# Kernel tuning notes

Hardware: AMD Instinct MI355X
Metric: run time of the kernel (lower is better)

## Reference

```python
import jax, jax.numpy as jnp
import numpy as np

B, S, E = 8, 2048, 2048   # batch, items, embedding_width
H, Dh = 16, 128           # head_width, head_embeddings (E = H*Dh)
M = 1024                  # memory_width


def setup_inputs() -> dict:
    key = jax.random.key(0)
    ks = jax.random.split(key, 9)
    scale_e = 1.0 / np.sqrt(E)
    scale_d = 1.0 / np.sqrt(Dh)
    return {
        "tensor": jax.random.normal(ks[0], (B, S, E), dtype=jnp.float32),
        # Query: Linear(E -> [H, Dh])
        "Wq": jax.random.normal(ks[1], (E, H, Dh), dtype=jnp.float32) * scale_e,
        "bq": jnp.zeros((H, Dh), dtype=jnp.float32),
        # trainable key/value banks + calibration (kaiming-uniform-like init)
        "key_params": (jax.random.uniform(ks[2], (H, M, Dh), dtype=jnp.float32) * 2 - 1) * np.sqrt(6.0 / Dh),
        "calibration": jnp.zeros((H, M, Dh), dtype=jnp.float32),
        "value": (jax.random.uniform(ks[3], (H, M, Dh), dtype=jnp.float32) * 2 - 1) * np.sqrt(6.0 / Dh),
        # Dehead: Linear([H, Dh] -> E)
        "Wd": jax.random.normal(ks[4], (H, Dh, E), dtype=jnp.float32) * scale_d,
        "bd": jnp.zeros((E,), dtype=jnp.float32),
    }


def reference(tensor, Wq, bq, key_params, calibration, value, Wd, bd):
    # query projection to heads: (B,S,E) -> (B,H,S,Dh) (fuses transpose(-2,-3))
    q = jnp.einsum("bse,ehd->bhsd", tensor, Wq) + bq[:, None, :]
    # eval-mode dropout is identity; key = KeyParameters + CalibrationBuffer
    k = key_params + calibration                      # (H,M,Dh)
    # scores scaled by sqrt(FULL embedding width), per the source
    score = jnp.einsum("bhsd,hmd->bhsm", q, k) / jnp.sqrt(jnp.float32(E))
    attn = jax.nn.softmax(score, axis=-1)             # (B,H,S,M)
    out = jnp.einsum("bhsm,hmd->bhsd", attn, value)   # (B,H,S,Dh)
    # dehead: (B,H,S,Dh) -> (B,S,E)
    return jnp.einsum("bhsd,hde->bse", out, Wd) + bd
```

## Files before the change

kernel.cpp:

```cpp
#include <hip/hip_runtime.h>
#include <stdint.h>

#define B_ 8
#define S_ 2048
#define E_ 2048
#define H_ 16
#define DH_ 128
#define M_ 1024
#define K_ 2048

typedef float f32x4 __attribute__((ext_vector_type(4)));
typedef float f32x16 __attribute__((ext_vector_type(16)));
typedef __bf16 bf16x8 __attribute__((ext_vector_type(8)));
typedef unsigned short ushort8 __attribute__((ext_vector_type(8)));
typedef unsigned short ushort4v __attribute__((ext_vector_type(4)));
typedef unsigned int uint4v __attribute__((ext_vector_type(4)));
typedef float float4v __attribute__((ext_vector_type(4)));

static __device__ __forceinline__ unsigned short f2bf(float f) {
  unsigned int u = __builtin_bit_cast(unsigned int, f);
  u += 0x7fffu + ((u >> 16) & 1u);
  return (unsigned short)(u >> 16);
}

static __device__ __forceinline__ float exp2f_fast(float x) {
#if __has_builtin(__builtin_amdgcn_exp2f)
  return __builtin_amdgcn_exp2f(x);
#else
  return __expf(x * 0.6931471805599453f);
#endif
}

static __device__ __forceinline__ f32x4 mfma16(ushort8 a, ushort8 b, f32x4 c) {
  return __builtin_amdgcn_mfma_f32_16x16x32_bf16(
      __builtin_bit_cast(bf16x8, a), __builtin_bit_cast(bf16x8, b), c, 0, 0, 0);
}

static __device__ __forceinline__ f32x16 mfma32(ushort8 a, ushort8 b, f32x16 c) {
  return __builtin_amdgcn_mfma_f32_32x32x16_bf16(
      __builtin_bit_cast(bf16x8, a), __builtin_bit_cast(bf16x8, b), c, 0, 0, 0);
}

static __device__ __forceinline__ void gload_lds16(const void* g, void* l) {
  __builtin_amdgcn_global_load_lds(
      (const __attribute__((address_space(1))) unsigned int*)g,
      (__attribute__((address_space(3))) unsigned int*)l, 16, 0, 0);
}


__global__ void cvt_bf16(const float* __restrict__ in, unsigned short* __restrict__ out, int n4) {
  int i = blockIdx.x * blockDim.x + threadIdx.x;
  int stride = gridDim.x * blockDim.x;
  for (; i < n4; i += stride) {
    float4v v = ((const float4v*)in)[i];
    ushort4v o;
    o[0] = f2bf(v[0]); o[1] = f2bf(v[1]); o[2] = f2bf(v[2]); o[3] = f2bf(v[3]);
    ((ushort4v*)out)[i] = o;
  }
}

__global__ void addcvt_bf16(const float* __restrict__ a, const float* __restrict__ b,
                            unsigned short* __restrict__ out, int n4) {
  int i = blockIdx.x * blockDim.x + threadIdx.x;
  int stride = gridDim.x * blockDim.x;
  for (; i < n4; i += stride) {
    float4v va = ((const float4v*)a)[i];
    float4v vb = ((const float4v*)b)[i];
    ushort4v o;
    o[0] = f2bf(va[0] + vb[0]); o[1] = f2bf(va[1] + vb[1]);
    o[2] = f2bf(va[2] + vb[2]); o[3] = f2bf(va[3] + vb[3]);
    ((ushort4v*)out)[i] = o;
  }
}

__global__ __launch_bounds__(256) void transpose_cvt(const float* __restrict__ in,
                                                     unsigned short* __restrict__ out,
                                                     int R, int C) {
  __shared__ float t[64][65];
  const int tx = threadIdx.x & 63, ty = threadIdx.x >> 6;
  const size_t base = (size_t)blockIdx.z * R * C;
  const int r0 = blockIdx.y * 64, c0 = blockIdx.x * 64;
#pragma unroll
  for (int i = 0; i < 64; i += 4)
    t[i + ty][tx] = in[base + (size_t)(r0 + i + ty) * C + (c0 + tx)];
  __syncthreads();
#pragma unroll
  for (int i = 0; i < 64; i += 4)
    out[base + (size_t)(c0 + i + ty) * R + (r0 + tx)] = f2bf(t[tx][i + ty]);
}

template <int EPI>
__global__ __launch_bounds__(512, 2) void gemm8p(const unsigned short* __restrict__ A,
                                                 const unsigned short* __restrict__ BT,
                                                 const float* __restrict__ bias,
                                                 void* __restrict__ Cout) {
  __shared__ __align__(16) unsigned short a_lds[2][2][8192];
  __shared__ __align__(16) unsigned short b_lds[2][2][8192];
  const int tid = threadIdx.x;
  const int w = tid >> 6, lane = tid & 63;
  const int l16 = lane & 15, l4 = lane >> 4;
  const int wr = w >> 2, wc = w & 3;
  const int bid = blockIdx.x;
  const int n0 = (bid & 7) << 8;
  const int m0 = (bid >> 3) << 8;

  const int rp0 = tid >> 3, gg0 = tid & 7, s0 = gg0 ^ (rp0 & 7);
  const int srow = rp0 * 2 + (s0 >> 2), sg = s0 & 3;
  const unsigned short* pA = A + (size_t)(m0 + srow) * K_ + sg * 8;
  const unsigned short* pB = BT + (size_t)(n0 + srow) * K_ + sg * 8;
  const int laneG = ((l16 >> 1) * 8 + (((l16 & 1) * 4 + l4) ^ ((l16 >> 1) & 7))) * 8;

  f32x4 acc[8][4];
#pragma unroll
  for (int i = 0; i < 8; ++i)
#pragma unroll
    for (int j = 0; j < 4; ++j) acc[i][j] = (f32x4)(0.f);

  ushort8 aF[4], bF[4];

#define STG(dst, srcp, T, kh)                                                \
  do {                                                                       \
    const unsigned short* s_ = (srcp) + (T) * 64 + (kh) * 32;                \
    gload_lds16(s_, &(dst)[tid * 8]);                                        \
    gload_lds16(s_ + (size_t)128 * K_, &(dst)[(512 + tid) * 8]);             \
  } while (0)

#define LDA(mg, buf, ks)                                                     \
  do {                                                                       \
    _Pragma("unroll") for (int mf = 0; mf < 4; ++mf)                         \
      aF[mf] = *(const ushort8*)&a_lds[buf][ks]                              \
          [(wr * 512 + ((mg) * 4 + mf) * 64) * 8 + laneG];                   \
  } while (0)

#define LDB(buf, ks)                                                         \
  do {                                                                       \
    _Pragma("unroll") for (int nf = 0; nf < 4; ++nf)                         \
      bF[nf] = *(const ushort8*)&b_lds[buf][ks]                              \
          [(wc * 256 + nf * 64) * 8 + laneG];                                \
  } while (0)

#define MM(mg)                                                               \
  do {                                                                       \
    __builtin_amdgcn_s_setprio(1);                                           \
    _Pragma("unroll") for (int mf = 0; mf < 4; ++mf)                         \
      _Pragma("unroll") for (int nf = 0; nf < 4; ++nf)                       \
        acc[(mg) * 4 + mf][nf] = mfma16(aF[mf], bF[nf], acc[(mg) * 4 + mf][nf]); \
    __builtin_amdgcn_s_setprio(0);                                           \
  } while (0)

#define NOVM ((void)0)
#define VMC6 asm volatile("s_waitcnt vmcnt(6)" ::: "memory")
#define VMC0 asm volatile("s_waitcnt vmcnt(0)" ::: "memory")

#define PHASE(mg, ks, buf, LOADB, STAGE, VM)                                 \
  do {                                                                       \
    if (LOADB) { LDB(buf, ks); }                                             \
    LDA(mg, buf, ks);                                                        \
    STAGE;                                                                   \
    __builtin_amdgcn_s_barrier();                                            \
    asm volatile("s_waitcnt lgkmcnt(0)" ::: "memory");                       \
    __builtin_amdgcn_sched_barrier(0);                                       \
    MM(mg);                                                                  \
    VM;                                                                      \
    __builtin_amdgcn_s_barrier();                                            \
  } while (0)

  STG(a_lds[0][0], pA, 0, 0);
  STG(b_lds[0][0], pB, 0, 0);
  STG(a_lds[0][1], pA, 0, 1);
  STG(b_lds[0][1], pB, 0, 1);
  STG(b_lds[1][0], pB, 1, 0);
  STG(a_lds[1][0], pA, 1, 0);
  STG(b_lds[1][1], pB, 1, 1);
  __builtin_amdgcn_sched_barrier(0);
  VMC6;
  __builtin_amdgcn_s_barrier();
  __builtin_amdgcn_sched_barrier(0);

#pragma unroll 1
  for (int i = 0; i < 15; ++i) {
    const int t1 = 2 * i + 1, t2 = 2 * i + 2, t3 = 2 * i + 3;
    PHASE(0, 0, 0, 1, STG(a_lds[1][1], pA, t1, 1), NOVM);
    PHASE(1, 0, 0, 0, STG(b_lds[0][0], pB, t2, 0), NOVM);
    PHASE(1, 1, 0, 1, STG(a_lds[0][0], pA, t2, 0), NOVM);
    PHASE(0, 1, 0, 0, STG(b_lds[0][1], pB, t2, 1), VMC6);
    PHASE(0, 0, 1, 1, STG(a_lds[0][1], pA, t2, 1), NOVM);
    PHASE(1, 0, 1, 0, STG(b_lds[1][0], pB, t3, 0), NOVM);
    PHASE(1, 1, 1, 1, STG(a_lds[1][0], pA, t3, 0), NOVM);
    PHASE(0, 1, 1, 0, STG(b_lds[1][1], pB, t3, 1), VMC6);
  }
  PHASE(0, 0, 0, 1, STG(a_lds[1][1], pA, 31, 1), NOVM);
  PHASE(1, 0, 0, 0, NOVM, NOVM);
  PHASE(1, 1, 0, 1, NOVM, NOVM);
  PHASE(0, 1, 0, 0, NOVM, VMC0);
  PHASE(0, 0, 1, 1, NOVM, NOVM);
  PHASE(1, 0, 1, 0, NOVM, NOVM);
  PHASE(1, 1, 1, 1, NOVM, NOVM);
  PHASE(0, 1, 1, 0, NOVM, NOVM);

#undef PHASE
#undef STG
#undef LDA
#undef LDB
#undef MM

#pragma unroll
  for (int mf = 0; mf < 8; ++mf) {
    const int mb = m0 + wr * 128 + mf * 16 + l4 * 4;
#pragma unroll
    for (int nf = 0; nf < 4; ++nf) {
      const int n = n0 + wc * 64 + nf * 16 + l16;
      const float bv = bias[n];
#pragma unroll
      for (int r = 0; r < 4; ++r) {
        const float v = acc[mf][nf][r] + bv;
        const int m = mb + r;
        if (EPI == 0) {
          const int b = m >> 11, s = m & 2047, h = n >> 7, d = n & 127;
          ((unsigned short*)Cout)[(((size_t)(b * 16 + h) << 11) + s) * 128 + d] =
              f2bf(v * 0.031879358f);
        } else {
          ((float*)Cout)[(size_t)m * E_ + n] = v;
        }
      }
    }
  }
}

__global__ __launch_bounds__(512, 2) void attn32(const unsigned short* __restrict__ Qb,
                                                 const unsigned short* __restrict__ Kb,
                                                 const unsigned short* __restrict__ VT,
                                                 unsigned short* __restrict__ Ob) {
  const int bh = blockIdx.x, b = bh >> 4, h = bh & 15;
  const int tid = threadIdx.x, wv = tid >> 6, lane = tid & 63;
  const int l32 = lane & 31, hi = lane >> 5;
  const int s_glob = blockIdx.y * 256 + wv * 32 + l32;

  __shared__ __align__(16) unsigned short k_sm[2][64 * 128];
  __shared__ __align__(16) unsigned short v_sm[2][128 * 64];
  __shared__ float inv_lds[8][32];

  const unsigned short* Kh = Kb + (size_t)h * M_ * DH_;
  const unsigned short* Vh = VT + (size_t)h * DH_ * M_;

  ushort8 qf[8];
  {
    const unsigned short* qrow = Qb + ((size_t)(b * 16 + h) * S_ + s_glob) * DH_ + hi * 8;
#pragma unroll
    for (int dc = 0; dc < 8; ++dc) qf[dc] = *(const ushort8*)(qrow + dc * 16);
  }

  f32x16 oacc[4];
#pragma unroll
  for (int dt = 0; dt < 4; ++dt) oacc[dt] = (f32x16)(0.f);
  float lsum = 0.f;

#define ASTAGE(buf, ch)                                                        \
  do {                                                                         \
    const int m0_ = (ch) << 6;                                                 \
    _Pragma("unroll") for (int j_ = 0; j_ < 2; ++j_) {                         \
      const int t_ = j_ * 512 + tid;                                           \
      const int m_ = t_ >> 4, p_ = t_ & 15;                                    \
      gload_lds16(Kh + (size_t)(m0_ + m_) * DH_ + ((p_ ^ (m_ & 7)) << 3),      \
                  &k_sm[buf][t_ * 8]);                                         \
    }                                                                          \
    _Pragma("unroll") for (int j_ = 0; j_ < 2; ++j_) {                         \
      const int t_ = j_ * 512 + tid;                                           \
      const int d_ = t_ >> 3, p_ = t_ & 7;                                     \
      gload_lds16(Vh + (size_t)d_ * M_ + m0_ + ((p_ ^ (d_ & 7)) << 3),         \
                  &v_sm[buf][t_ * 8]);                                         \
    }                                                                          \
  } while (0)

  int cur = 0;
  ASTAGE(0, 0);
  __syncthreads();

  for (int c = 0; c < 16; ++c) {
    if (c < 15) ASTAGE(cur ^ 1, c + 1);

    f32x16 sacc[2];
    sacc[0] = (f32x16)(0.f);
    sacc[1] = (f32x16)(0.f);
#pragma unroll
    for (int mb = 0; mb < 2; ++mb) {
      const int m_ = mb * 32 + l32;
      const unsigned short* kr = &k_sm[cur][m_ * 128];
      __builtin_amdgcn_s_setprio(1);
#pragma unroll
      for (int dc = 0; dc < 8; ++dc) {
        ushort8 kf = *(const ushort8*)(kr + (((dc * 2 + hi) ^ (m_ & 7)) << 3));
        sacc[mb] = mfma32(kf, qf[dc], sacc[mb]);
      }
      __builtin_amdgcn_s_setprio(0);
    }

#pragma unroll
    for (int mb = 0; mb < 2; ++mb) {
      float pe[16];
#pragma unroll
      for (int r = 0; r < 16; ++r) {
        pe[r] = exp2f_fast(sacc[mb][r]);
        lsum += pe[r];
      }
      ushort8 pa[2];
#pragma unroll
      for (int mk = 0; mk < 2; ++mk) {
        const int o = mk * 8;
        unsigned x0, x1, y0, y1;
        asm("v_cvt_pk_bf16_f32 %0, %1, %2" : "=v"(x0) : "v"(pe[o + 0]), "v"(pe[o + 1]));
        asm("v_cvt_pk_bf16_f32 %0, %1, %2" : "=v"(x1) : "v"(pe[o + 2]), "v"(pe[o + 3]));
        asm("v_cvt_pk_bf16_f32 %0, %1, %2" : "=v"(y0) : "v"(pe[o + 4]), "v"(pe[o + 5]));
        asm("v_cvt_pk_bf16_f32 %0, %1, %2" : "=v"(y1) : "v"(pe[o + 6]), "v"(pe[o + 7]));
        asm("v_permlane32_swap_b32 %0, %1" : "+v"(x0), "+v"(y0));
        asm("v_permlane32_swap_b32 %0, %1" : "+v"(x1), "+v"(y1));
        uint4v pw;
        pw[0] = x0; pw[1] = x1; pw[2] = y0; pw[3] = y1;
        pa[mk] = __builtin_bit_cast(ushort8, pw);
      }
#pragma unroll
      for (int dt = 0; dt < 4; ++dt) {
        const int d_ = dt * 32 + l32;
        const unsigned short* vr = &v_sm[cur][d_ * 64];
        __builtin_amdgcn_s_setprio(1);
#pragma unroll
        for (int mk = 0; mk < 2; ++mk) {
          const int gv = mb * 4 + mk * 2 + hi;
          ushort8 vf = *(const ushort8*)(vr + ((gv ^ (d_ & 7)) << 3));
          oacc[dt] = mfma32(pa[mk], vf, oacc[dt]);
        }
        __builtin_amdgcn_s_setprio(0);
      }
    }
    __syncthreads();
    cur ^= 1;
  }
#undef ASTAGE

  float tot = lsum + __shfl_xor(lsum, 32, 64);
  if (hi == 0) inv_lds[wv][l32] = 1.0f / tot;
#pragma unroll
  for (int r = 0; r < 16; ++r) {
    const int srow = (r & 3) + 8 * (r >> 2) + 4 * hi;
    const float iv = inv_lds[wv][srow];
    unsigned short* orow =
        Ob + ((size_t)b * S_ + (size_t)(blockIdx.y * 256 + wv * 32 + srow)) * (H_ * DH_) +
        h * DH_ + l32;
#pragma unroll
    for (int dt = 0; dt < 4; ++dt) {
      const float val = oacc[dt][r] * iv;
      unsigned u;
      asm("v_cvt_pk_bf16_f32 %0, %1, %2" : "=v"(u) : "v"(val), "v"(val));
      orow[dt * 32] = (unsigned short)u;
    }
  }
}


extern "C" void kernel_launch(void* const* d_in, const int* in_sizes, int n_in,
                              void* d_out, int out_size, void* d_ws, size_t ws_size,
                              hipStream_t stream) {
  const float* X   = (const float*)d_in[0];
  const float* Wq  = (const float*)d_in[1];
  const float* bq  = (const float*)d_in[2];
  const float* Kp  = (const float*)d_in[3];
  const float* Cal = (const float*)d_in[4];
  const float* V   = (const float*)d_in[5];
  const float* Wd  = (const float*)d_in[6];
  const float* bd  = (const float*)d_in[7];

  char* ws = (char*)d_ws;
  unsigned short* Xbf = (unsigned short*)(ws + 0);
  unsigned short* Ob  = Xbf;
  unsigned short* Qb  = (unsigned short*)(ws + 67108864);
  unsigned short* WqT = (unsigned short*)(ws + 134217728);
  unsigned short* WdT = (unsigned short*)(ws + 142606336);
  unsigned short* Kb  = (unsigned short*)(ws + 150994944);
  unsigned short* VT  = (unsigned short*)(ws + 155189248);

  cvt_bf16<<<2048, 256, 0, stream>>>(X, Xbf, (B_ * S_ * E_) / 4);
  addcvt_bf16<<<1024, 256, 0, stream>>>(Kp, Cal, Kb, (H_ * M_ * DH_) / 4);
  transpose_cvt<<<dim3(E_ / 64, E_ / 64, 1), 256, 0, stream>>>(Wq, WqT, E_, H_ * DH_);
  transpose_cvt<<<dim3(E_ / 64, E_ / 64, 1), 256, 0, stream>>>(Wd, WdT, H_ * DH_, E_);
  transpose_cvt<<<dim3(DH_ / 64, M_ / 64, H_), 256, 0, stream>>>(V, VT, M_, DH_);

  gemm8p<0><<<dim3(512), 512, 0, stream>>>(Xbf, WqT, bq, Qb);

  attn32<<<dim3(B_ * H_, S_ / 256), 512, 0, stream>>>(Qb, Kb, VT, Ob);

  gemm8p<1><<<dim3(512), 512, 0, stream>>>(Ob, WdT, bd, (float*)d_out);
}
```

Before: 475.2 us.

## Process two 32-row query tiles per wave in attention to reuse K/V fragments

The attention kernel now runs 256 threads per block, and each wave handles 64 query rows as two 32-row sub-tiles, so every K and V fragment read from LDS feeds two MFMAs instead of one. The K/V staging layout is changed to a fragment-ordered, lane-contiguous arrangement without XOR swizzle, so each lane's 16-byte read is a direct contiguous access. The QK, softmax and PV steps are interleaved per 32-column block. This halves LDS read traffic per MFMA but doubles the accumulator and query registers per wave, which may reduce occupancy or cause spills. Fewer waves per block also leave less latency hiding.

```diff
diff --git a/kernel.cpp b/kernel.cpp
--- a/kernel.cpp
+++ b/kernel.cpp
@@ -227,49 +227,56 @@
   }
 }
 
-__global__ __launch_bounds__(512, 2) void attn32(const unsigned short* __restrict__ Qb,
+__global__ __launch_bounds__(256, 2) void attn64(const unsigned short* __restrict__ Qb,
                                                  const unsigned short* __restrict__ Kb,
                                                  const unsigned short* __restrict__ VT,
                                                  unsigned short* __restrict__ Ob) {
   const int bh = blockIdx.x, b = bh >> 4, h = bh & 15;
   const int tid = threadIdx.x, wv = tid >> 6, lane = tid & 63;
   const int l32 = lane & 31, hi = lane >> 5;
-  const int s_glob = blockIdx.y * 256 + wv * 32 + l32;
-
-  __shared__ __align__(16) unsigned short k_sm[2][64 * 128];
-  __shared__ __align__(16) unsigned short v_sm[2][128 * 64];
-  __shared__ float inv_lds[8][32];
+
+  __shared__ __align__(16) unsigned short k_sm[2][16 * 512];
+  __shared__ __align__(16) unsigned short v_sm[2][16 * 512];
+  __shared__ float inv_lds[4][2][32];
 
   const unsigned short* Kh = Kb + (size_t)h * M_ * DH_;
   const unsigned short* Vh = VT + (size_t)h * DH_ * M_;
 
-  ushort8 qf[8];
-  {
-    const unsigned short* qrow = Qb + ((size_t)(b * 16 + h) * S_ + s_glob) * DH_ + hi * 8;
-#pragma unroll
-    for (int dc = 0; dc < 8; ++dc) qf[dc] = *(const ushort8*)(qrow + dc * 16);
-  }
-
-  f32x16 oacc[4];
-#pragma unroll
-  for (int dt = 0; dt < 4; ++dt) oacc[dt] = (f32x16)(0.f);
-  float lsum = 0.f;
-
-#define ASTAGE(buf, ch)                                                        \
-  do {                                                                         \
-    const int m0_ = (ch) << 6;                                                 \
-    _Pragma("unroll") for (int j_ = 0; j_ < 2; ++j_) {                         \
-      const int t_ = j_ * 512 + tid;                                           \
-      const int m_ = t_ >> 4, p_ = t_ & 15;                                    \
-      gload_lds16(Kh + (size_t)(m0_ + m_) * DH_ + ((p_ ^ (m_ & 7)) << 3),      \
-                  &k_sm[buf][t_ * 8]);                                         \
-    }                                                                          \
-    _Pragma("unroll") for (int j_ = 0; j_ < 2; ++j_) {                         \
-      const int t_ = j_ * 512 + tid;                                           \
-      const int d_ = t_ >> 3, p_ = t_ & 7;                                     \
-      gload_lds16(Vh + (size_t)d_ * M_ + m0_ + ((p_ ^ (d_ & 7)) << 3),         \
-                  &v_sm[buf][t_ * 8]);                                         \
-    }                                                                          \
+  ushort8 qf[2][8];
+#pragma unroll
+  for (int sub = 0; sub < 2; ++sub) {
+    const int srow = blockIdx.y * 256 + wv * 64 + sub * 32 + l32;
+    const unsigned short* qrow = Qb + ((size_t)(b * 16 + h) * S_ + srow) * DH_ + hi * 8;
+#pragma unroll
+    for (int dc = 0; dc < 8; ++dc) qf[sub][dc] = *(const ushort8*)(qrow + dc * 16);
+  }
+
+  f32x16 oacc[2][4];
+#pragma unroll
+  for (int sub = 0; sub < 2; ++sub)
+#pragma unroll
+    for (int dt = 0; dt < 4; ++dt) oacc[sub][dt] = (f32x16)(0.f);
+  float lsum[2] = {0.f, 0.f};
+
+#define ASTAGE(buf, ch)                                                         \
+  do {                                                                          \
+    const int m0c = (ch) << 6;                                                  \
+    _Pragma("unroll") for (int j_ = 0; j_ < 4; ++j_) {                          \
+      const int L_ = j_ * 256 + tid;                                            \
+      const int st_ = L_ >> 6, g_ = L_ & 63;                                    \
+      const int mb_ = st_ >> 3, dc_ = st_ & 7;                                  \
+      const int pt_ = g_ >> 5, rw_ = g_ & 31;                                   \
+      gload_lds16(Kh + (size_t)(m0c + mb_ * 32 + rw_) * DH_ + dc_ * 16 + pt_ * 8, \
+                  &k_sm[buf][L_ * 8]);                                          \
+    }                                                                           \
+    _Pragma("unroll") for (int j_ = 0; j_ < 4; ++j_) {                          \
+      const int L_ = j_ * 256 + tid;                                            \
+      const int st_ = L_ >> 6, g_ = L_ & 63;                                    \
+      const int dt_ = st_ >> 2, mb_ = (st_ >> 1) & 1, mk_ = st_ & 1;            \
+      const int pt_ = g_ >> 5, rw_ = g_ & 31;                                   \
+      gload_lds16(Vh + (size_t)(dt_ * 32 + rw_) * M_ + m0c + mb_ * 32 + mk_ * 16 + pt_ * 8, \
+                  &v_sm[buf][L_ * 8]);                                          \
+    }                                                                           \
   } while (0)
 
   int cur = 0;
@@ -279,81 +286,84 @@
   for (int c = 0; c < 16; ++c) {
     if (c < 15) ASTAGE(cur ^ 1, c + 1);
 
-    f32x16 sacc[2];
-    sacc[0] = (f32x16)(0.f);
-    sacc[1] = (f32x16)(0.f);
 #pragma unroll
     for (int mb = 0; mb < 2; ++mb) {
-      const int m_ = mb * 32 + l32;
-      const unsigned short* kr = &k_sm[cur][m_ * 128];
+      f32x16 sacc0 = (f32x16)(0.f), sacc1 = (f32x16)(0.f);
       __builtin_amdgcn_s_setprio(1);
 #pragma unroll
       for (int dc = 0; dc < 8; ++dc) {
-        ushort8 kf = *(const ushort8*)(kr + (((dc * 2 + hi) ^ (m_ & 7)) << 3));
-        sacc[mb] = mfma32(kf, qf[dc], sacc[mb]);
+        ushort8 kf = *(const ushort8*)&k_sm[cur][((mb * 8 + dc) * 64 + lane) * 8];
+        sacc0 = mfma32(kf, qf[0][dc], sacc0);
+        sacc1 = mfma32(kf, qf[1][dc], sacc1);
+      }
+      __builtin_amdgcn_s_setprio(0);
+
+      ushort8 pa[2][2];
+#pragma unroll
+      for (int sub = 0; sub < 2; ++sub) {
+        float pe[16];
+#pragma unroll
+        for (int r = 0; r < 16; ++r) {
+          pe[r] = exp2f_fast(sub == 0 ? sacc0[r] : sacc1[r]);
+          lsum[sub] += pe[r];
+        }
+#pragma unroll
+        for (int mk = 0; mk < 2; ++mk) {
+          const int o = mk * 8;
+          unsigned x0, x1, y0, y1;
+          asm("v_cvt_pk_bf16_f32 %0, %1, %2" : "=v"(x0) : "v"(pe[o + 0]), "v"(pe[o + 1]));
+          asm("v_cvt_pk_bf16_f32 %0, %1, %2" : "=v"(x1) : "v"(pe[o + 2]), "v"(pe[o + 3]));
+          asm("v_cvt_pk_bf16_f32 %0, %1, %2" : "=v"(y0) : "v"(pe[o + 4]), "v"(pe[o + 5]));
+          asm("v_cvt_pk_bf16_f32 %0, %1, %2" : "=v"(y1) : "v"(pe[o + 6]), "v"(pe[o + 7]));
+          asm("v_permlane32_swap_b32 %0, %1" : "+v"(x0), "+v"(y0));
+          asm("v_permlane32_swap_b32 %0, %1" : "+v"(x1), "+v"(y1));
+          uint4v pw;
+          pw[0] = x0; pw[1] = x1; pw[2] = y0; pw[3] = y1;
+          pa[sub][mk] = __builtin_bit_cast(ushort8, pw);
+        }
+      }
+
+      __builtin_amdgcn_s_setprio(1);
+#pragma unroll
+      for (int dt = 0; dt < 4; ++dt) {
+#pragma unroll
+        for (int mk = 0; mk < 2; ++mk) {
+          ushort8 vf = *(const ushort8*)&v_sm[cur][((dt * 4 + mb * 2 + mk) * 64 + lane) * 8];
+          oacc[0][dt] = mfma32(pa[0][mk], vf, oacc[0][dt]);
+          oacc[1][dt] = mfma32(pa[1][mk], vf, oacc[1][dt]);
+        }
       }
       __builtin_amdgcn_s_setprio(0);
     }
-
-#pragma unroll
-    for (int mb = 0; mb < 2; ++mb) {
-      float pe[16];
-#pragma unroll
-      for (int r = 0; r < 16; ++r) {
-        pe[r] = exp2f_fast(sacc[mb][r]);
-        lsum += pe[r];
-      }
-      ushort8 pa[2];
-#pragma unroll
-      for (int mk = 0; mk < 2; ++mk) {
-        const int o = mk * 8;
-        unsigned x0, x1, y0, y1;
-        asm("v_cvt_pk_bf16_f32 %0, %1, %2" : "=v"(x0) : "v"(pe[o + 0]), "v"(pe[o + 1]));
-        asm("v_cvt_pk_bf16_f32 %0, %1, %2" : "=v"(x1) : "v"(pe[o + 2]), "v"(pe[o + 3]));
-        asm("v_cvt_pk_bf16_f32 %0, %1, %2" : "=v"(y0) : "v"(pe[o + 4]), "v"(pe[o + 5]));
-        asm("v_cvt_pk_bf16_f32 %0, %1, %2" : "=v"(y1) : "v"(pe[o + 6]), "v"(pe[o + 7]));
-        asm("v_permlane32_swap_b32 %0, %1" : "+v"(x0), "+v"(y0));
-        asm("v_permlane32_swap_b32 %0, %1" : "+v"(x1), "+v"(y1));
-        uint4v pw;
-        pw[0] = x0; pw[1] = x1; pw[2] = y0; pw[3] = y1;
-        pa[mk] = __builtin_bit_cast(ushort8, pw);
-      }
+    __syncthreads();
+    cur ^= 1;
+  }
+#undef ASTAGE
+
+#pragma unroll
+  for (int sub = 0; sub < 2; ++sub) {
+    float tot = lsum[sub] + __shfl_xor(lsum[sub], 32, 64);
+    if (hi == 0) inv_lds[wv][sub][l32] = 1.0f / tot;
+  }
+  __builtin_amdgcn_s_barrier();
+#pragma unroll
+  for (int sub = 0; sub < 2; ++sub)
+#pragma unroll
+    for (int r = 0; r < 16; ++r) {
+      const int crow = (r & 3) + 8 * (r >> 2) + 4 * hi;
+      const float iv = inv_lds[wv][sub][crow];
+      unsigned short* orow =
+          Ob + ((size_t)b * S_ + (size_t)(blockIdx.y * 256 + wv * 64 + sub * 32 + crow)) *
+                   (H_ * DH_) +
+          h * DH_ + l32;
 #pragma unroll
       for (int dt = 0; dt < 4; ++dt) {
-        const int d_ = dt * 32 + l32;
-        const unsigned short* vr = &v_sm[cur][d_ * 64];
-        __builtin_amdgcn_s_setprio(1);
-#pragma unroll
-        for (int mk = 0; mk < 2; ++mk) {
-          const int gv = mb * 4 + mk * 2 + hi;
-          ushort8 vf = *(const ushort8*)(vr + ((gv ^ (d_ & 7)) << 3));
-          oacc[dt] = mfma32(pa[mk], vf, oacc[dt]);
-        }
-        __builtin_amdgcn_s_setprio(0);
+        const float val = oacc[sub][dt][r] * iv;
+        unsigned u;
+        asm("v_cvt_pk_bf16_f32 %0, %1, %2" : "=v"(u) : "v"(val), "v"(val));
+        orow[dt * 32] = (unsigned short)u;
       }
     }
-    __syncthreads();
-    cur ^= 1;
-  }
-#undef ASTAGE
-
-  float tot = lsum + __shfl_xor(lsum, 32, 64);
-  if (hi == 0) inv_lds[wv][l32] = 1.0f / tot;
-#pragma unroll
-  for (int r = 0; r < 16; ++r) {
-    const int srow = (r & 3) + 8 * (r >> 2) + 4 * hi;
-    const float iv = inv_lds[wv][srow];
-    unsigned short* orow =
-        Ob + ((size_t)b * S_ + (size_t)(blockIdx.y * 256 + wv * 32 + srow)) * (H_ * DH_) +
-        h * DH_ + l32;
-#pragma unroll
-    for (int dt = 0; dt < 4; ++dt) {
-      const float val = oacc[dt][r] * iv;
-      unsigned u;
-      asm("v_cvt_pk_bf16_f32 %0, %1, %2" : "=v"(u) : "v"(val), "v"(val));
-      orow[dt * 32] = (unsigned short)u;
-    }
-  }
 }
 
 
@@ -386,7 +396,7 @@
 
   gemm8p<0><<<dim3(512), 512, 0, stream>>>(Xbf, WqT, bq, Qb);
 
-  attn32<<<dim3(B_ * H_, S_ / 256), 512, 0, stream>>>(Qb, Kb, VT, Ob);
+  attn64<<<dim3(B_ * H_, S_ / 256), 256, 0, stream>>>(Qb, Kb, VT, Ob);
 
   gemm8p<1><<<dim3(512), 512, 0, stream>>>(Ob, WdT, bd, (float*)d_out);
 }
```

Result: slower. 567.4 us (+19.4%).
